# Performance work log

Hardware: AMD Instinct MI355X
Metric: run time of the kernel (lower is better)

The kernel has to match this reference:

```python
import jax, jax.numpy as jnp
import numpy as np
from math import sqrt

B, S, E, H = 4, 2048, 1024, 16
D = E // H  # per-head dim = 64


def setup_inputs() -> dict:
    key = jax.random.key(0)
    ks = jax.random.split(key, 11)
    f = lambda k, shape, scale=1.0: jax.random.normal(k, shape, dtype=jnp.float32) * scale
    return {
        "Q": f(ks[0], (B, S, E)),
        "K": f(ks[1], (B, S, E)),
        "V": f(ks[2], (B, S, E)),
        "Wq": f(ks[3], (E, E), 1.0 / sqrt(E)),
        "bq": f(ks[4], (E,), 0.02),
        "Wk": f(ks[5], (E, E), 1.0 / sqrt(E)),
        "bk": f(ks[6], (E,), 0.02),
        "Wv": f(ks[7], (E, E), 1.0 / sqrt(E)),
        "bv": f(ks[8], (E,), 0.02),
        "Wo": f(ks[9], (E, E), 1.0 / sqrt(E)),
        "bo": f(ks[10], (E,), 0.02),
    }


def reference(Q, K, V, Wq, bq, Wk, bk, Wv, bv, Wo, bo):
    # Linear projections (torch Linear: x @ W.T + b)
    q = Q @ Wq.T + bq  # [B,S,E]
    k = K @ Wk.T + bk
    v = V @ Wv.T + bv
    # torch.chunk along last dim into H heads == reshape [B,S,H,D]
    q = q.reshape(B, S, H, D)
    k = k.reshape(B, S, H, D)
    v = v.reshape(B, S, H, D)
    scale = 1.0 / sqrt(D)
    # batched-over-heads scaled dot-product attention
    scores = jnp.einsum("bqhd,bkhd->bhqk", q, k) * scale  # [B,H,S,S]
    attn = jax.nn.softmax(scores, axis=-1)
    out = jnp.einsum("bhqk,bkhd->bqhd", attn, v).reshape(B, S, E)
    # dropout p=0.0 -> identity
    return out @ Wo.T + bo
```

## Files before the change

kernel.cpp:

```cpp
#include <hip/hip_runtime.h>
#include <hip/hip_bf16.h>

#define B_SZ   4
#define S_LEN  2048
#define E_DIM  1024
#define H_NUM  16
#define D_DIM  64
#define M_ROWS (B_SZ * S_LEN)
#define QK_SCALE 0.1803368801111204f

typedef __attribute__((ext_vector_type(8))) __bf16 bf16x8;
typedef __attribute__((ext_vector_type(4))) float  f32x4;

__device__ __forceinline__ bf16x8 load8(const void* p) {
    return __builtin_bit_cast(bf16x8, *reinterpret_cast<const uint4*>(p));
}

#if defined(__has_builtin)
#if __has_builtin(__builtin_amdgcn_exp2f)
#define EXP2F(x) __builtin_amdgcn_exp2f(x)
#endif
#if __has_builtin(__builtin_amdgcn_global_load_lds)
#define HAVE_GLL 1
#endif
#endif
#ifndef EXP2F
#define EXP2F(x) exp2f(x)
#endif

__device__ __forceinline__ void stage16(const __hip_bfloat16* g, __hip_bfloat16* lbase, int lane) {
#ifdef HAVE_GLL
    __builtin_amdgcn_global_load_lds((const __attribute__((address_space(1))) unsigned int*)g,
                                     (__attribute__((address_space(3))) unsigned int*)lbase,
                                     16, 0, 0);
#else
    reinterpret_cast<uint4*>(lbase)[lane] = *reinterpret_cast<const uint4*>(g);
#endif
}

#define N8A (1 << 20)
#define N8W (1 << 17)
#define N8TOT (3 * N8A + 4 * N8W)

struct CvtArgs {
    const float* s[7];
    __hip_bfloat16* d[7];
};

__global__ __launch_bounds__(256) void cvt_all(CvtArgs a)
{
    const int i = blockIdx.x * 256 + threadIdx.x;
    if (i >= N8TOT) return;
    int seg, off;
    if (i < 3 * N8A) { seg = i >> 20;              off = i & (N8A - 1); }
    else             { const int j = i - 3 * N8A;
                       seg = 3 + (j >> 17);        off = j & (N8W - 1); }
    const float* s = a.s[seg];
    __hip_bfloat16* d = a.d[seg];
    const float4 x = reinterpret_cast<const float4*>(s)[off * 2];
    const float4 y = reinterpret_cast<const float4*>(s)[off * 2 + 1];
    __hip_bfloat16 o[8];
    o[0] = __float2bfloat16(x.x); o[1] = __float2bfloat16(x.y);
    o[2] = __float2bfloat16(x.z); o[3] = __float2bfloat16(x.w);
    o[4] = __float2bfloat16(y.x); o[5] = __float2bfloat16(y.y);
    o[6] = __float2bfloat16(y.z); o[7] = __float2bfloat16(y.w);
    reinterpret_cast<uint4*>(d)[off] = *reinterpret_cast<uint4*>(o);
}

__global__ __launch_bounds__(256) void cvt_f32_bf16(const float* __restrict__ s,
                                                    __hip_bfloat16* __restrict__ d,
                                                    int n8)
{
    const int i = blockIdx.x * 256 + threadIdx.x;
    if (i >= n8) return;
    const float4 a = reinterpret_cast<const float4*>(s)[i * 2];
    const float4 b = reinterpret_cast<const float4*>(s)[i * 2 + 1];
    __hip_bfloat16 o[8];
    o[0] = __float2bfloat16(a.x); o[1] = __float2bfloat16(a.y);
    o[2] = __float2bfloat16(a.z); o[3] = __float2bfloat16(a.w);
    o[4] = __float2bfloat16(b.x); o[5] = __float2bfloat16(b.y);
    o[6] = __float2bfloat16(b.z); o[7] = __float2bfloat16(b.w);
    reinterpret_cast<uint4*>(d)[i] = *reinterpret_cast<uint4*>(o);
}

struct GemmArgs {
    const __hip_bfloat16* A[3];
    const __hip_bfloat16* W[3];
    const float* bias[3];
    void* C[3];
    float scale[3];
    int mode[3];
    int nper;
};

__global__ __launch_bounds__(512, 2) void gemm_bt(GemmArgs g)
{
    __shared__ __attribute__((aligned(16))) char lds[2][65536];

    const int tid = threadIdx.x;
    const int wid = tid >> 6, lane = tid & 63;
    const int quad = lane >> 4, l16 = lane & 15;
    const int wm = wid >> 2, wn = wid & 3;

    const int cpx = gridDim.x >> 3;
    const int id  = (blockIdx.x & 7) * cpx + (blockIdx.x >> 3);
    const int seg = id / g.nper;
    const int bid = id % g.nper;
    const int bm = bid >> 2, bn = bid & 3;
    const int row0 = bm * 256, col0 = bn * 256;

    const __hip_bfloat16* A = g.A[seg];
    const __hip_bfloat16* W = g.W[seg];

    const int srow = tid >> 3;
    const int sgk  = (tid & 7) ^ (srow & 7);
    const __hip_bfloat16* aSrc = A + (size_t)(row0 + srow) * E_DIM + sgk * 8;
    const __hip_bfloat16* bSrc = W + (size_t)(col0 + srow) * E_DIM + sgk * 8;
    const int stW = wid << 10;

    const int abase = (wm * 128 + l16) * 128;
    const int bbase = 32768 + (wn * 64 + l16) * 128;
    const int sl0 = ((quad)     ^ (l16 & 7)) << 4;
    const int sl1 = ((quad | 4) ^ (l16 & 7)) << 4;

    f32x4 acc[8][4];
    const f32x4 zero = {0.f, 0.f, 0.f, 0.f};
#pragma unroll
    for (int i = 0; i < 8; i++)
#pragma unroll
        for (int j = 0; j < 4; j++) acc[i][j] = zero;

    auto stage = [&](int t, int c) {
        char* d = lds[t & 1];
        stage16(aSrc + (size_t)c * 64 * E_DIM + t * 64,
                (__hip_bfloat16*)(d + c * 8192 + stW), lane);
        stage16(bSrc + (size_t)c * 64 * E_DIM + t * 64,
                (__hip_bfloat16*)(d + 32768 + c * 8192 + stW), lane);
    };

#define PHASE_TAIL()                                             \
    __builtin_amdgcn_s_barrier();                                \
    asm volatile("s_waitcnt lgkmcnt(0)" ::: "memory");           \
    __builtin_amdgcn_sched_barrier(0);                           \
    __builtin_amdgcn_s_setprio(1);

#define PHASE_END()                                              \
    __builtin_amdgcn_s_setprio(0);                               \
    __builtin_amdgcn_s_barrier();

    const int NT = E_DIM / 64;
    stage(0, 0); stage(0, 1); stage(0, 2); stage(0, 3);
    for (int t = 0; t < NT; ++t) {
        const bool pf = (t + 1 < NT);
        const char* base = lds[t & 1];
        if (pf) { stage(t + 1, 0); stage(t + 1, 1);
                  asm volatile("s_waitcnt vmcnt(4)" ::: "memory"); }
        else    { asm volatile("s_waitcnt vmcnt(0)" ::: "memory"); }
        __builtin_amdgcn_s_barrier();

        bf16x8 af[4], bf[4];
#pragma unroll
        for (int j = 0; j < 4; j++) bf[j] = load8(base + bbase + j * 2048 + sl0);
#pragma unroll
        for (int i = 0; i < 4; i++) af[i] = load8(base + abase + i * 2048 + sl0);
        PHASE_TAIL()
#pragma unroll
        for (int i = 0; i < 4; i++)
#pragma unroll
            for (int j = 0; j < 4; j++)
                acc[i][j] = __builtin_amdgcn_mfma_f32_16x16x32_bf16(af[i], bf[j], acc[i][j], 0, 0, 0);
        PHASE_END()
#pragma unroll
        for (int i = 0; i < 4; i++) af[i] = load8(base + abase + (i + 4) * 2048 + sl0);
        if (pf) stage(t + 1, 2);
        PHASE_TAIL()
#pragma unroll
        for (int i = 0; i < 4; i++)
#pragma unroll
            for (int j = 0; j < 4; j++)
                acc[i + 4][j] = __builtin_amdgcn_mfma_f32_16x16x32_bf16(af[i], bf[j], acc[i + 4][j], 0, 0, 0);
        PHASE_END()
#pragma unroll
        for (int j = 0; j < 4; j++) bf[j] = load8(base + bbase + j * 2048 + sl1);
#pragma unroll
        for (int i = 0; i < 4; i++) af[i] = load8(base + abase + i * 2048 + sl1);
        if (pf) stage(t + 1, 3);
        PHASE_TAIL()
#pragma unroll
        for (int i = 0; i < 4; i++)
#pragma unroll
            for (int j = 0; j < 4; j++)
                acc[i][j] = __builtin_amdgcn_mfma_f32_16x16x32_bf16(af[i], bf[j], acc[i][j], 0, 0, 0);
        PHASE_END()
#pragma unroll
        for (int i = 0; i < 4; i++) af[i] = load8(base + abase + (i + 4) * 2048 + sl1);
        PHASE_TAIL()
#pragma unroll
        for (int i = 0; i < 4; i++)
#pragma unroll
            for (int j = 0; j < 4; j++)
                acc[i + 4][j] = __builtin_amdgcn_mfma_f32_16x16x32_bf16(af[i], bf[j], acc[i + 4][j], 0, 0, 0);
        PHASE_END()
    }
#undef PHASE_TAIL
#undef PHASE_END

    const int   mode  = g.mode[seg];
    const float scale = g.scale[seg];
    const float* bias = g.bias[seg];
    void* Cout        = g.C[seg];
#pragma unroll
    for (int j = 0; j < 4; j++) {
        const int col = col0 + wn * 64 + j * 16 + l16;
        const float bv = bias[col];
#pragma unroll
        for (int i = 0; i < 8; i++) {
            const int row = row0 + wm * 128 + i * 16 + quad * 4;
            if (mode == 3) {
                __attribute__((aligned(8))) __hip_bfloat16 o[4];
#pragma unroll
                for (int r = 0; r < 4; r++) o[r] = __float2bfloat16((acc[i][j][r] + bv) * scale);
                const int b_ = row >> 11, s_ = row & 2047, h_ = col >> 6, d_ = col & 63;
                *reinterpret_cast<uint2*>((__hip_bfloat16*)Cout +
                    (((size_t)(b_ * H_NUM + h_)) << 17) + (d_ << 11) + s_) =
                    *reinterpret_cast<uint2*>(o);
            } else {
#pragma unroll
                for (int r = 0; r < 4; r++) {
                    const float v = (acc[i][j][r] + bv) * scale;
                    const int rr = row + r;
                    if (mode == 0) {
                        ((__hip_bfloat16*)Cout)[(size_t)rr * E_DIM + col] = __float2bfloat16(v);
                    } else if (mode == 1) {
                        ((float*)Cout)[(size_t)rr * E_DIM + col] = v;
                    } else {
                        const int b_ = rr >> 11, s_ = rr & 2047, h_ = col >> 6, d_ = col & 63;
                        ((__hip_bfloat16*)Cout)[(((size_t)(b_ * H_NUM + h_)) << 17) + (s_ << 6) + d_] =
                            __float2bfloat16(v);
                    }
                }
            }
        }
    }
}

__global__ __launch_bounds__(512) void attn(const __hip_bfloat16* __restrict__ Qt,
                                            const __hip_bfloat16* __restrict__ Kt,
                                            const __hip_bfloat16* __restrict__ Vt,
                                            __hip_bfloat16* __restrict__ Op)
{
    __shared__ __hip_bfloat16 Pls[8][64][40];
    __shared__ __attribute__((aligned(16))) __hip_bfloat16 Kls[2][32 * 64];
    __shared__ __attribute__((aligned(16))) __hip_bfloat16 Vls[2][64 * 32];

    const int x = blockIdx.x;
    const int bh     = (x & 7) * 8 + ((x >> 3) & 7);
    const int qchunk = x >> 6;
    const int tid = threadIdx.x;
    const int wave = tid >> 6, lane = tid & 63;
    const int quad = lane >> 4, l16 = lane & 15;
    const int qrow0 = qchunk * 512 + wave * 64;

    const __hip_bfloat16* qb = Qt + ((size_t)bh << 17);
    const __hip_bfloat16* kb = Kt + ((size_t)bh << 17);
    const __hip_bfloat16* vb = Vt + ((size_t)bh << 17);
    __hip_bfloat16* pw = &Pls[wave][0][0];

    const int rt = tid & 255;
    const int skey = rt >> 3, sgk = (rt & 7) ^ (skey & 7);
    const __hip_bfloat16* kSrc = kb + (skey << 6) + (sgk << 3);
    const int sd = rt >> 2, sgv = (rt & 3) ^ ((sd >> 1) & 3);
    const __hip_bfloat16* vSrc = vb + ((size_t)sd << 11) + (sgv << 3);
    const int stW = (wave & 3) << 10;

    const int ksw = l16 & 7, vsw = (l16 >> 1) & 3;

    bf16x8 qf[4][2];
#pragma unroll
    for (int qt = 0; qt < 4; qt++) {
        qf[qt][0] = load8(qb + ((qrow0 + qt * 16 + l16) << 6) + quad * 8);
        qf[qt][1] = load8(qb + ((qrow0 + qt * 16 + l16) << 6) + 32 + quad * 8);
    }

    const f32x4 zero = {0.f, 0.f, 0.f, 0.f};
    f32x4 o_acc[4][4];
#pragma unroll
    for (int qt = 0; qt < 4; qt++)
#pragma unroll
        for (int dj = 0; dj < 4; dj++) o_acc[qt][dj] = zero;
    float lsum[4] = {0.f, 0.f, 0.f, 0.f};

    auto stageKV = [&](int kv, int b) {
        if (tid < 256)
            stage16(kSrc + (kv << 6), (__hip_bfloat16*)((char*)&Kls[b][0] + stW), lane);
        else
            stage16(vSrc + kv,        (__hip_bfloat16*)((char*)&Vls[b][0] + stW), lane);
    };

    auto compute = [&](int b) {
        const char* Kbuf = (const char*)&Kls[b][0];
        const char* Vbuf = (const char*)&Vls[b][0];
#pragma unroll
        for (int t = 0; t < 2; t++) {
            const bf16x8 ka = load8(Kbuf + ((t * 16 + l16) << 7) + ((quad ^ ksw) << 4));
            const bf16x8 kc = load8(Kbuf + ((t * 16 + l16) << 7) + (((quad + 4) ^ ksw) << 4));
#pragma unroll
            for (int qt = 0; qt < 4; qt++) {
                f32x4 st = __builtin_amdgcn_mfma_f32_16x16x32_bf16(ka, qf[qt][0], zero, 0, 0, 0);
                st       = __builtin_amdgcn_mfma_f32_16x16x32_bf16(kc, qf[qt][1], st, 0, 0, 0);
                const float p0 = EXP2F(st[0]), p1 = EXP2F(st[1]);
                const float p2 = EXP2F(st[2]), p3 = EXP2F(st[3]);
                lsum[qt] += (p0 + p1) + (p2 + p3);
                const unsigned u0 = (unsigned)__bfloat16_as_ushort(__float2bfloat16(p0));
                const unsigned u1 = (unsigned)__bfloat16_as_ushort(__float2bfloat16(p1));
                const unsigned u2 = (unsigned)__bfloat16_as_ushort(__float2bfloat16(p2));
                const unsigned u3 = (unsigned)__bfloat16_as_ushort(__float2bfloat16(p3));
                uint2 w;
                w.x = (u1 << 16) | u0;
                w.y = (u3 << 16) | u2;
                *reinterpret_cast<uint2*>(&pw[(qt * 16 + l16) * 40 + t * 16 + quad * 4]) = w;
            }
        }
        bf16x8 vf[4];
#pragma unroll
        for (int dj = 0; dj < 4; dj++)
            vf[dj] = load8(Vbuf + ((dj * 16 + l16) << 6) + ((quad ^ vsw) << 4));
        __builtin_amdgcn_s_setprio(1);
#pragma unroll
        for (int qt = 0; qt < 4; qt++) {
            const bf16x8 pa = load8(&pw[(qt * 16 + l16) * 40 + quad * 8]);
#pragma unroll
            for (int dj = 0; dj < 4; dj++)
                o_acc[qt][dj] = __builtin_amdgcn_mfma_f32_16x16x32_bf16(pa, vf[dj], o_acc[qt][dj], 0, 0, 0);
        }
        __builtin_amdgcn_s_setprio(0);
    };

    stageKV(0, 0);
    int cur = 0;
    for (int kv0 = 0; kv0 < S_LEN; kv0 += 32) {
        __syncthreads();
        if (kv0 + 32 < S_LEN) stageKV(kv0 + 32, cur ^ 1);
        compute(cur);
        cur ^= 1;
    }

    const int b_ = bh >> 4, h_ = bh & 15;
#pragma unroll
    for (int qt = 0; qt < 4; qt++) {
        float l = lsum[qt];
        l += __shfl_xor(l, 16, 64);
        l += __shfl_xor(l, 32, 64);
#pragma unroll
        for (int r = 0; r < 4; r++) {
            const float lr = __shfl(l, quad * 4 + r, 64);
            const float inv = 1.f / lr;
            const size_t ro = ((size_t)b_ * S_LEN + (qrow0 + qt * 16 + quad * 4 + r)) * E_DIM + h_ * D_DIM;
#pragma unroll
            for (int dj = 0; dj < 4; dj++)
                Op[ro + dj * 16 + l16] = __float2bfloat16(o_acc[qt][dj][r] * inv);
        }
    }
}

extern "C" void kernel_launch(void* const* d_in, const int* in_sizes, int n_in,
                              void* d_out, int out_size, void* d_ws, size_t ws_size,
                              hipStream_t stream)
{
    const float* Qf  = (const float*)d_in[0];
    const float* Kf  = (const float*)d_in[1];
    const float* Vf  = (const float*)d_in[2];
    const float* Wqf = (const float*)d_in[3];
    const float* bqf = (const float*)d_in[4];
    const float* Wkf = (const float*)d_in[5];
    const float* bkf = (const float*)d_in[6];
    const float* Wvf = (const float*)d_in[7];
    const float* bvf = (const float*)d_in[8];
    const float* Wof = (const float*)d_in[9];
    const float* bof = (const float*)d_in[10];

    const size_t n_act = (size_t)M_ROWS * E_DIM;
    const size_t n_w   = (size_t)E_DIM * E_DIM;

    const dim3 blk(256), gblk(512), ablk(512);
    const int cg_act = (int)(n_act / 8 / 256);
    const int cg_w   = (int)(n_w / 8 / 256);

    const size_t need_fast = (6 * n_act + 4 * n_w) * sizeof(__hip_bfloat16);

    if (ws_size >= need_fast) {
        __hip_bfloat16* Xq = (__hip_bfloat16*)d_ws;
        __hip_bfloat16* Xk = Xq + n_act;
        __hip_bfloat16* Xv = Xk + n_act;
        __hip_bfloat16* Wb = Xv + n_act;
        __hip_bfloat16* Qt = Wb + 4 * n_w;
        __hip_bfloat16* Kt = Qt + n_act;
        __hip_bfloat16* Vt = Kt + n_act;

        CvtArgs ca;
        ca.s[0] = Qf;  ca.s[1] = Kf;  ca.s[2] = Vf;
        ca.s[3] = Wqf; ca.s[4] = Wkf; ca.s[5] = Wvf; ca.s[6] = Wof;
        ca.d[0] = Xq;  ca.d[1] = Xk;  ca.d[2] = Xv;
        ca.d[3] = Wb;  ca.d[4] = Wb + n_w; ca.d[5] = Wb + 2 * n_w; ca.d[6] = Wb + 3 * n_w;
        cvt_all<<<dim3(N8TOT / 256), blk, 0, stream>>>(ca);

        GemmArgs qkv;
        qkv.A[0] = Xq;  qkv.A[1] = Xk;  qkv.A[2] = Xv;
        qkv.W[0] = Wb;  qkv.W[1] = Wb + n_w;  qkv.W[2] = Wb + 2*n_w;
        qkv.bias[0] = bqf;  qkv.bias[1] = bkf;  qkv.bias[2] = bvf;
        qkv.C[0] = Qt;  qkv.C[1] = Kt;  qkv.C[2] = Vt;
        qkv.scale[0] = QK_SCALE;  qkv.scale[1] = 1.0f;  qkv.scale[2] = 1.0f;
        qkv.mode[0] = 2;  qkv.mode[1] = 2;  qkv.mode[2] = 3;
        qkv.nper = 128;
        gemm_bt<<<dim3(384), gblk, 0, stream>>>(qkv);

        attn<<<dim3(256), ablk, 0, stream>>>(Qt, Kt, Vt, Xq);

        GemmArgs og;
        og.A[0] = Xq;  og.A[1] = Xq;  og.A[2] = Xq;
        og.W[0] = Wb + 3*n_w;  og.W[1] = og.W[0];  og.W[2] = og.W[0];
        og.bias[0] = bof;  og.bias[1] = bof;  og.bias[2] = bof;
        og.C[0] = d_out;  og.C[1] = d_out;  og.C[2] = d_out;
        og.scale[0] = 1.0f;  og.scale[1] = 1.0f;  og.scale[2] = 1.0f;
        og.mode[0] = 1;  og.mode[1] = 1;  og.mode[2] = 1;
        og.nper = 128;
        gemm_bt<<<dim3(128), gblk, 0, stream>>>(og);
    } else {
        __hip_bfloat16* X  = (__hip_bfloat16*)d_ws;
        __hip_bfloat16* Wb = X + n_act;
        __hip_bfloat16* Qt = Wb + n_w;
        __hip_bfloat16* Kt = Qt + n_act;
        __hip_bfloat16* Vt = Kt + n_act;

        auto one = [&](const float* Af, const float* Wf, const float* bf_,
                       void* C, float sc, int md) {
            cvt_f32_bf16<<<cg_act, blk, 0, stream>>>(Af, X, (int)(n_act / 8));
            cvt_f32_bf16<<<cg_w,   blk, 0, stream>>>(Wf, Wb, (int)(n_w / 8));
            GemmArgs a;
            a.A[0] = X; a.A[1] = X; a.A[2] = X;
            a.W[0] = Wb; a.W[1] = Wb; a.W[2] = Wb;
            a.bias[0] = bf_; a.bias[1] = bf_; a.bias[2] = bf_;
            a.C[0] = C; a.C[1] = C; a.C[2] = C;
            a.scale[0] = sc; a.scale[1] = sc; a.scale[2] = sc;
            a.mode[0] = md; a.mode[1] = md; a.mode[2] = md;
            a.nper = 128;
            gemm_bt<<<dim3(128), gblk, 0, stream>>>(a);
        };
        one(Qf, Wqf, bqf, Qt, QK_SCALE, 2);
        one(Kf, Wkf, bkf, Kt, 1.0f, 2);
        one(Vf, Wvf, bvf, Vt, 1.0f, 3);
        attn<<<dim3(256), ablk, 0, stream>>>(Qt, Kt, Vt, X);
        cvt_f32_bf16<<<cg_w, blk, 0, stream>>>(Wof, Wb, (int)(n_w / 8));
        GemmArgs og;
        og.A[0] = X; og.A[1] = X; og.A[2] = X;
        og.W[0] = Wb; og.W[1] = Wb; og.W[2] = Wb;
        og.bias[0] = bof; og.bias[1] = bof; og.bias[2] = bof;
        og.C[0] = d_out; og.C[1] = d_out; og.C[2] = d_out;
        og.scale[0] = 1.0f; og.scale[1] = 1.0f; og.scale[2] = 1.0f;
        og.mode[0] = 1; og.mode[1] = 1; og.mode[2] = 1;
        og.nper = 128;
        gemm_bt<<<dim3(128), gblk, 0, stream>>>(og);
    }
}
```

Baseline: 370.1 us.

## Add smaller-tile output GEMM and split attention into 256-thread blocks

Adds a new output-projection GEMM that uses 128x256 tiles with a three-stage LDS pipeline, so it launches 256 blocks instead of 128 and fills more CUs. The attention kernel now uses 256-thread blocks over 256-row query chunks, launching 512 blocks, and every thread stages both K and V. The aim is better occupancy and load balance for the output GEMM and the attention kernel. The trade-off is more K/V re-reads per head and more per-block overhead.

Result: faster. 354.0 us (-4.4%).

```diff
diff --git a/kernel.cpp b/kernel.cpp
--- a/kernel.cpp
+++ b/kernel.cpp
@@ -93,7 +93,7 @@
     int nper;
 };
 
-__global__ __launch_bounds__(512, 2) void gemm_bt(GemmArgs g)
+__global__ __launch_bounds__(512, 2) void gemm_qkv(GemmArgs g)
 {
     __shared__ __attribute__((aligned(16))) char lds[2][65536];
 
@@ -244,34 +244,147 @@
     }
 }
 
-__global__ __launch_bounds__(512) void attn(const __hip_bfloat16* __restrict__ Qt,
+__global__ __launch_bounds__(512, 4) void gemm_og(GemmArgs g)
+{
+    __shared__ __attribute__((aligned(16))) char lds_raw[3 * 24576];
+
+    const int tid = threadIdx.x;
+    const int wid = tid >> 6, lane = tid & 63;
+    const int quad = lane >> 4, l16 = lane & 15;
+    const int wm = wid >> 2, wn = wid & 3;
+
+    const int seg = blockIdx.x >> 8;
+    int bid = blockIdx.x & 255;
+    bid = (bid & 7) * 32 + (bid >> 3);
+    const int bm = bid >> 2, bn = bid & 3;
+    const int row0 = bm * 128, col0 = bn * 256;
+
+    const __hip_bfloat16* A = g.A[seg];
+    const __hip_bfloat16* W = g.W[seg];
+
+    const int s_line = tid >> 3, s_gr = tid & 7;
+    const int glin  = s_gr ^ (s_line & 7);
+    const int s_row = (s_line << 1) + (glin >> 2);
+    const int s_ks  = glin & 3;
+    const __hip_bfloat16* gA = A + (size_t)(row0 + s_row) * E_DIM + s_ks * 8;
+    const __hip_bfloat16* gB = W + (size_t)(col0 + s_row) * E_DIM + s_ks * 8;
+    const int stA = wid << 10;
+
+    const int rg   = (((l16 & 1) << 2) | quad) ^ ((l16 >> 1) & 7);
+    const int aoff = (wm * 32 + (l16 >> 1)) * 128 + rg * 16;
+    const int boff = (wn * 32 + (l16 >> 1)) * 128 + rg * 16;
+
+    f32x4 acc[4][4];
+    const f32x4 zero = {0.f, 0.f, 0.f, 0.f};
+#pragma unroll
+    for (int i = 0; i < 4; i++)
+#pragma unroll
+        for (int j = 0; j < 4; j++) acc[i][j] = zero;
+
+    auto stage_t = [&](int t) {
+        char* b = lds_raw + (t % 3) * 24576;
+        const int ko = t * 32;
+        stage16(gA + ko, (__hip_bfloat16*)(b + stA), lane);
+        stage16(gB + ko, (__hip_bfloat16*)(b + 8192 + stA), lane);
+        stage16(gB + (size_t)128 * E_DIM + ko, (__hip_bfloat16*)(b + 16384 + stA), lane);
+    };
+
+    auto body = [&](int t, bool stg) {
+        __builtin_amdgcn_s_barrier();
+        __builtin_amdgcn_sched_barrier(0);
+        if (stg) stage_t(t + 2);
+        const char* ab = lds_raw + (t % 3) * 24576;
+        bf16x8 af[4], bf[4];
+#pragma unroll
+        for (int i = 0; i < 4; i++) af[i] = load8(ab + aoff + i * 1024);
+#pragma unroll
+        for (int j = 0; j < 4; j++) bf[j] = load8(ab + 8192 + boff + j * 1024);
+        __builtin_amdgcn_s_setprio(1);
+#pragma unroll
+        for (int i = 0; i < 4; i++)
+#pragma unroll
+            for (int j = 0; j < 4; j++)
+                acc[i][j] = __builtin_amdgcn_mfma_f32_16x16x32_bf16(af[i], bf[j], acc[i][j], 0, 0, 0);
+        __builtin_amdgcn_s_setprio(0);
+        __builtin_amdgcn_sched_barrier(0);
+    };
+
+    const int NT = E_DIM / 32;
+    stage_t(0); stage_t(1);
+    for (int t = 0; t < NT - 2; ++t) {
+        asm volatile("s_waitcnt vmcnt(3)" ::: "memory");
+        body(t, true);
+    }
+    asm volatile("s_waitcnt vmcnt(3)" ::: "memory"); body(NT - 2, false);
+    asm volatile("s_waitcnt vmcnt(0)" ::: "memory"); body(NT - 1, false);
+
+    const int   mode  = g.mode[seg];
+    const float scale = g.scale[seg];
+    const float* bias = g.bias[seg];
+    void* Cout        = g.C[seg];
+#pragma unroll
+    for (int j = 0; j < 4; j++) {
+        const int col = col0 + wn * 64 + j * 16 + l16;
+        const float bv = bias[col];
+#pragma unroll
+        for (int i = 0; i < 4; i++) {
+            const int row = row0 + wm * 64 + i * 16 + quad * 4;
+            if (mode == 3) {
+                __attribute__((aligned(8))) __hip_bfloat16 o[4];
+#pragma unroll
+                for (int r = 0; r < 4; r++) o[r] = __float2bfloat16((acc[i][j][r] + bv) * scale);
+                const int b_ = row >> 11, s_ = row & 2047, h_ = col >> 6, d_ = col & 63;
+                *reinterpret_cast<uint2*>((__hip_bfloat16*)Cout +
+                    (((size_t)(b_ * H_NUM + h_)) << 17) + (d_ << 11) + s_) =
+                    *reinterpret_cast<uint2*>(o);
+            } else {
+#pragma unroll
+                for (int r = 0; r < 4; r++) {
+                    const float v = (acc[i][j][r] + bv) * scale;
+                    const int rr = row + r;
+                    if (mode == 0) {
+                        ((__hip_bfloat16*)Cout)[(size_t)rr * E_DIM + col] = __float2bfloat16(v);
+                    } else if (mode == 1) {
+                        ((float*)Cout)[(size_t)rr * E_DIM + col] = v;
+                    } else {
+                        const int b_ = rr >> 11, s_ = rr & 2047, h_ = col >> 6, d_ = col & 63;
+                        ((__hip_bfloat16*)Cout)[(((size_t)(b_ * H_NUM + h_)) << 17) + (s_ << 6) + d_] =
+                            __float2bfloat16(v);
+                    }
+                }
+            }
+        }
+    }
+}
+
+__global__ __launch_bounds__(256) void attn(const __hip_bfloat16* __restrict__ Qt,
                                             const __hip_bfloat16* __restrict__ Kt,
                                             const __hip_bfloat16* __restrict__ Vt,
                                             __hip_bfloat16* __restrict__ Op)
 {
-    __shared__ __hip_bfloat16 Pls[8][64][40];
+    __shared__ __hip_bfloat16 Pls[4][64][40];
     __shared__ __attribute__((aligned(16))) __hip_bfloat16 Kls[2][32 * 64];
     __shared__ __attribute__((aligned(16))) __hip_bfloat16 Vls[2][64 * 32];
 
     const int x = blockIdx.x;
-    const int bh     = (x & 7) * 8 + ((x >> 3) & 7);
-    const int qchunk = x >> 6;
+    const int xcd = x & 7, idx = x >> 3;
+    const int bh     = xcd * 8 + (idx & 7);
+    const int qchunk = idx >> 3;
     const int tid = threadIdx.x;
     const int wave = tid >> 6, lane = tid & 63;
     const int quad = lane >> 4, l16 = lane & 15;
-    const int qrow0 = qchunk * 512 + wave * 64;
+    const int qrow0 = qchunk * 256 + wave * 64;
 
     const __hip_bfloat16* qb = Qt + ((size_t)bh << 17);
     const __hip_bfloat16* kb = Kt + ((size_t)bh << 17);
     const __hip_bfloat16* vb = Vt + ((size_t)bh << 17);
     __hip_bfloat16* pw = &Pls[wave][0][0];
 
-    const int rt = tid & 255;
-    const int skey = rt >> 3, sgk = (rt & 7) ^ (skey & 7);
+    const int skey = tid >> 3, sgk = (tid & 7) ^ (skey & 7);
     const __hip_bfloat16* kSrc = kb + (skey << 6) + (sgk << 3);
-    const int sd = rt >> 2, sgv = (rt & 3) ^ ((sd >> 1) & 3);
+    const int sd = tid >> 2, sgv = (tid & 3) ^ ((sd >> 1) & 3);
     const __hip_bfloat16* vSrc = vb + ((size_t)sd << 11) + (sgv << 3);
-    const int stW = (wave & 3) << 10;
+    const int stW = wave << 10;
 
     const int ksw = l16 & 7, vsw = (l16 >> 1) & 3;
 
@@ -291,10 +404,8 @@
     float lsum[4] = {0.f, 0.f, 0.f, 0.f};
 
     auto stageKV = [&](int kv, int b) {
-        if (tid < 256)
-            stage16(kSrc + (kv << 6), (__hip_bfloat16*)((char*)&Kls[b][0] + stW), lane);
-        else
-            stage16(vSrc + kv,        (__hip_bfloat16*)((char*)&Vls[b][0] + stW), lane);
+        stage16(kSrc + (kv << 6), (__hip_bfloat16*)((char*)&Kls[b][0] + stW), lane);
+        stage16(vSrc + kv,        (__hip_bfloat16*)((char*)&Vls[b][0] + stW), lane);
     };
 
     auto compute = [&](int b) {
@@ -382,7 +493,7 @@
     const size_t n_act = (size_t)M_ROWS * E_DIM;
     const size_t n_w   = (size_t)E_DIM * E_DIM;
 
-    const dim3 blk(256), gblk(512), ablk(512);
+    const dim3 blk(256), gblk(512), ablk(256);
     const int cg_act = (int)(n_act / 8 / 256);
     const int cg_w   = (int)(n_w / 8 / 256);
 
@@ -412,9 +523,9 @@
         qkv.scale[0] = QK_SCALE;  qkv.scale[1] = 1.0f;  qkv.scale[2] = 1.0f;
         qkv.mode[0] = 2;  qkv.mode[1] = 2;  qkv.mode[2] = 3;
         qkv.nper = 128;
-        gemm_bt<<<dim3(384), gblk, 0, stream>>>(qkv);
-
-        attn<<<dim3(256), ablk, 0, stream>>>(Qt, Kt, Vt, Xq);
+        gemm_qkv<<<dim3(384), gblk, 0, stream>>>(qkv);
+
+        attn<<<dim3(512), ablk, 0, stream>>>(Qt, Kt, Vt, Xq);
 
         GemmArgs og;
         og.A[0] = Xq;  og.A[1] = Xq;  og.A[2] = Xq;
@@ -423,8 +534,8 @@
         og.C[0] = d_out;  og.C[1] = d_out;  og.C[2] = d_out;
         og.scale[0] = 1.0f;  og.scale[1] = 1.0f;  og.scale[2] = 1.0f;
         og.mode[0] = 1;  og.mode[1] = 1;  og.mode[2] = 1;
-        og.nper = 128;
-        gemm_bt<<<dim3(128), gblk, 0, stream>>>(og);
+        og.nper = 256;
+        gemm_og<<<dim3(256), gblk, 0, stream>>>(og);
     } else {
         __hip_bfloat16* X  = (__hip_bfloat16*)d_ws;
         __hip_bfloat16* Wb = X + n_act;
@@ -443,13 +554,13 @@
             a.C[0] = C; a.C[1] = C; a.C[2] = C;
             a.scale[0] = sc; a.scale[1] = sc; a.scale[2] = sc;
             a.mode[0] = md; a.mode[1] = md; a.mode[2] = md;
-            a.nper = 128;
-            gemm_bt<<<dim3(128), gblk, 0, stream>>>(a);
+            a.nper = 256;
+            gemm_og<<<dim3(256), gblk, 0, stream>>>(a);
         };
         one(Qf, Wqf, bqf, Qt, QK_SCALE, 2);
         one(Kf, Wkf, bkf, Kt, 1.0f, 2);
         one(Vf, Wvf, bvf, Vt, 1.0f, 3);
-        attn<<<dim3(256), ablk, 0, stream>>>(Qt, Kt, Vt, X);
+        attn<<<dim3(512), ablk, 0, stream>>>(Qt, Kt, Vt, X);
         cvt_f32_bf16<<<cg_w, blk, 0, stream>>>(Wof, Wb, (int)(n_w / 8));
         GemmArgs og;
         og.A[0] = X; og.A[1] = X; og.A[2] = X;
@@ -458,7 +569,7 @@
         og.C[0] = d_out; og.C[1] = d_out; og.C[2] = d_out;
         og.scale[0] = 1.0f; og.scale[1] = 1.0f; og.scale[2] = 1.0f;
         og.mode[0] = 1; og.mode[1] = 1; og.mode[2] = 1;
-        og.nper = 128;
-        gemm_bt<<<dim3(128), gblk, 0, stream>>>(og);
-    }
-}
+        og.nper = 256;
+        gemm_og<<<dim3(256), gblk, 0, stream>>>(og);
+    }
+}
```
